# Kernel optimization log

Hardware: AMD Instinct MI355X
Metric: run time of the kernel (lower is better)

Reference implementation:

```python
import jax, jax.numpy as jnp
import numpy as np

B, L, D, H = 8, 1024, 512, 8  # L must equal len_ for the skew trick
DH = D // H


def setup_inputs() -> dict:
    key = jax.random.key(0)
    ks = jax.random.split(key, 6)
    s = 0.02
    return {
        "x": jax.random.normal(ks[0], (B, L, D), dtype=jnp.float32),
        "Wq": jax.random.normal(ks[1], (D, D), dtype=jnp.float32) * s,
        "Wk": jax.random.normal(ks[2], (D, D), dtype=jnp.float32) * s,
        "Wv": jax.random.normal(ks[3], (D, D), dtype=jnp.float32) * s,
        "We": jax.random.normal(ks[4], (L, DH), dtype=jnp.float32) * s,  # e_projection weight: (len_, d_head)
        "Wo": jax.random.normal(ks[5], (D, D), dtype=jnp.float32) * s,
        "bo": jnp.zeros((D,), dtype=jnp.float32),
        "unused": 0,
    }


def reference(x, Wq, Wk, Wv, We, Wo, bo, unused):
    Bx, Lx, Dx = x.shape
    q = (x @ Wq.T).reshape(Bx, Lx, H, DH)  # blhd
    k = (x @ Wk.T).reshape(Bx, Lx, H, DH)
    v = (x @ Wv.T).reshape(Bx, Lx, H, DH)

    # relative-position logits: e_projection(q) then permute -> (B, H, L, len_)
    qe = jnp.einsum('blhd,ed->bhle', q, We)

    # 'skew' trick: reflect-pad right by L-1, zero-pad (right 1, bottom L-1),
    # reshape (B,H,2L-1,2L) -> (B,H,2L,2L-1), slice [:L, L-1:] -> (B,H,L,L)
    qe = jnp.pad(qe, ((0, 0), (0, 0), (0, 0), (0, Lx - 1)), mode='reflect')
    qe = jnp.pad(qe, ((0, 0), (0, 0), (0, Lx - 1), (0, 1)))
    qe = qe.reshape(Bx, H, 2 * Lx, 2 * Lx - 1)
    s_rel = qe[:, :, :Lx, Lx - 1:]

    scale = 1.0 / jnp.sqrt(jnp.asarray(DH, dtype=x.dtype))
    scores = jnp.einsum('blhd,bshd->bhls', q, k)
    A = jax.nn.softmax(scale * (scores + s_rel), axis=-1)
    V = jnp.einsum('bhls,bshd->blhd', A, v).reshape(Bx, Lx, Dx)
    return V @ Wo.T + bo
```

## Files before the change

kernel.cpp:

```cpp
#include <hip/hip_runtime.h>

#define Lc 1024
#define Dc 512
#define Hc 8
#define DHc 64

typedef __attribute__((ext_vector_type(8))) short bf16x8;
typedef __attribute__((ext_vector_type(4))) float f32x4;

typedef __attribute__((address_space(1))) const unsigned int guint;
typedef __attribute__((address_space(3))) unsigned int luint;

__device__ __forceinline__ void gload_lds16(const void* g, void* l) {
    __builtin_amdgcn_global_load_lds((guint*)g, (luint*)l, 16, 0, 0);
}

__device__ __forceinline__ unsigned short f2bf(float f) {
    unsigned u = __float_as_uint(f);
    u += 0x7fffu + ((u >> 16) & 1u);
    return (unsigned short)(u >> 16);
}
__device__ __forceinline__ unsigned short f2bft(float f) {
    return (unsigned short)(__float_as_uint(f) >> 16);
}
__device__ __forceinline__ unsigned pk2(float a, float b) {
    return (unsigned)f2bf(a) | ((unsigned)f2bf(b) << 16);
}
__device__ __forceinline__ float bf2f(unsigned short s) { return __uint_as_float(((unsigned)s) << 16); }

__global__ void cvt_all_kernel(
    const float* __restrict__ x,  const float* __restrict__ Wq,
    const float* __restrict__ Wk, const float* __restrict__ Wv,
    const float* __restrict__ Wo, const float* __restrict__ We,
    unsigned short* __restrict__ xb,  unsigned short* __restrict__ wqb,
    unsigned short* __restrict__ wkb, unsigned short* __restrict__ wvb,
    unsigned short* __restrict__ wob, unsigned short* __restrict__ wet)
{
    int bid = blockIdx.x;
    const float* src; unsigned short* dst; size_t base;
    if      (bid < 4096) { src = x;  dst = xb;  base = (size_t)bid * 1024; }
    else if (bid < 4352) { src = Wq; dst = wqb; base = (size_t)(bid-4096) * 1024; }
    else if (bid < 4608) { src = Wk; dst = wkb; base = (size_t)(bid-4352) * 1024; }
    else if (bid < 4864) { src = Wv; dst = wvb; base = (size_t)(bid-4608) * 1024; }
    else if (bid < 5120) { src = Wo; dst = wob; base = (size_t)(bid-4864) * 1024; }
    else                 { src = We; dst = wet; base = (size_t)(bid-5120) * 1024; }
    size_t i = base + (size_t)threadIdx.x * 4;
    float4 a = *(const float4*)&src[i];
    *(uint2*)&dst[i] = make_uint2(pk2(a.x, a.y), pk2(a.z, a.w));
}

__global__ __launch_bounds__(256, 3) void proj_mfma_kernel(
    const unsigned short* __restrict__ xb,
    const unsigned short* __restrict__ wq, const unsigned short* __restrict__ wk,
    const unsigned short* __restrict__ wv,
    unsigned short* __restrict__ qo, unsigned short* __restrict__ ko,
    unsigned short* __restrict__ vtg, float qscale)
{
    const unsigned short* W;
    if (blockIdx.z == 0)      W = wq;
    else if (blockIdx.z == 1) W = wk;
    else                      W = wv;

    __shared__ unsigned short smem[128 * 136];
    unsigned short* As = smem;
    unsigned short* Bs = smem + 8192;

    const int t = threadIdx.x;
    const int lane = t & 63, w = t >> 6;
    const int lq = lane >> 4, ln = lane & 15;
    const int m0 = blockIdx.y * 128, n0 = blockIdx.x * 128;
    const int wm = (w & 1) * 64, wn = (w >> 1) * 64;
    const int srow = t >> 3;
    const int lsg  = ((t & 7) ^ ((t >> 3) & 7)) * 8;
    const int key  = ln & 7;

    f32x4 acc[4][4];
    #pragma unroll
    for (int i = 0; i < 4; i++)
        #pragma unroll
        for (int j = 0; j < 4; j++) acc[i][j] = (f32x4){0.f,0.f,0.f,0.f};

    for (int c0 = 0; c0 < 512; c0 += 64) {
        __syncthreads();
        #pragma unroll
        for (int g = 0; g < 4; g++) {
            gload_lds16(&xb[(size_t)(m0 + 32*g + srow) * 512 + c0 + lsg], &As[(32*g + srow)*64 + (t&7)*8]);
            gload_lds16(&W [(size_t)(n0 + 32*g + srow) * 512 + c0 + lsg], &Bs[(32*g + srow)*64 + (t&7)*8]);
        }
        __syncthreads();

        #pragma unroll
        for (int kk = 0; kk < 2; kk++) {
            bf16x8 af[4], bf[4];
            #pragma unroll
            for (int i = 0; i < 4; i++)
                af[i] = *(bf16x8*)&As[(wm + 16*i + ln)*64 + ((kk*4 + lq) ^ key)*8];
            #pragma unroll
            for (int j = 0; j < 4; j++)
                bf[j] = *(bf16x8*)&Bs[(wn + 16*j + ln)*64 + ((kk*4 + lq) ^ key)*8];
            #pragma unroll
            for (int i = 0; i < 4; i++)
                #pragma unroll
                for (int j = 0; j < 4; j++)
                    acc[i][j] = __builtin_amdgcn_mfma_f32_16x16x32_bf16(af[i], bf[j], acc[i][j], 0, 0, 0);
        }
    }

    if (blockIdx.z < 2) {
        unsigned short* out = (blockIdx.z == 0) ? qo : ko;
        const float osc = (blockIdx.z == 0) ? qscale : 1.0f;
        #pragma unroll
        for (int i = 0; i < 4; i++) {
            #pragma unroll
            for (int r = 0; r < 4; r++) {
                int m = m0 + wm + 16*i + 4*lq + r;
                int b = m >> 10, l = m & 1023;
                #pragma unroll
                for (int j = 0; j < 4; j++) {
                    int n = n0 + wn + 16*j + ln;
                    int h = n >> 6, dh = n & 63;
                    out[((size_t)((b*Hc + h)*Lc + l))*DHc + dh] = f2bf(acc[i][j][r] * osc);
                }
            }
        }
    } else {
        __syncthreads();
        unsigned short* Ts = smem;
        #pragma unroll
        for (int i = 0; i < 4; i++) {
            int mlb = wm + 16*i + 4*lq;
            #pragma unroll
            for (int j = 0; j < 4; j++) {
                int nl = wn + 16*j + ln;
                *(uint2*)&Ts[nl*136 + mlb] = make_uint2(pk2(acc[i][j][0], acc[i][j][1]),
                                                        pk2(acc[i][j][2], acc[i][j][3]));
            }
        }
        __syncthreads();
        const int b = m0 >> 10, l0m = m0 & 1023;
        const int nl = t >> 1, seg = (t & 1) * 64;
        const int ng = n0 + nl, h = ng >> 6, dh = ng & 63;
        unsigned short* dst = vtg + (((size_t)(b*Hc + h))*DHc + dh)*Lc + l0m + seg;
        #pragma unroll
        for (int u = 0; u < 8; u++)
            *(uint4*)&dst[8*u] = *(uint4*)&Ts[nl*136 + seg + 8*u];
    }
}

__global__ __launch_bounds__(256, 4) void out_mfma_kernel(
    const unsigned short* __restrict__ A, const unsigned short* __restrict__ W,
    const float* __restrict__ bias, float* __restrict__ out)
{
    __shared__ unsigned short As[64 * 64];
    __shared__ unsigned short Bs[64 * 64];

    const int t = threadIdx.x;
    const int lane = t & 63, w = t >> 6;
    const int lq = lane >> 4, ln = lane & 15;
    const int m0 = blockIdx.y * 64, n0 = blockIdx.x * 64;
    const int wm = (w & 1) * 32, wn = (w >> 1) * 32;
    const int srow = t >> 3;
    const int lsg  = ((t & 7) ^ ((t >> 3) & 7)) * 8;
    const int key  = ln & 7;

    f32x4 acc[2][2];
    #pragma unroll
    for (int i = 0; i < 2; i++)
        #pragma unroll
        for (int j = 0; j < 2; j++) acc[i][j] = (f32x4){0.f,0.f,0.f,0.f};

    for (int c0 = 0; c0 < 512; c0 += 64) {
        __syncthreads();
        #pragma unroll
        for (int g = 0; g < 2; g++) {
            gload_lds16(&A[(size_t)(m0 + 32*g + srow) * 512 + c0 + lsg], &As[(32*g + srow)*64 + (t&7)*8]);
            gload_lds16(&W[(size_t)(n0 + 32*g + srow) * 512 + c0 + lsg], &Bs[(32*g + srow)*64 + (t&7)*8]);
        }
        __syncthreads();

        #pragma unroll
        for (int kk = 0; kk < 2; kk++) {
            bf16x8 af[2], bf[2];
            #pragma unroll
            for (int i = 0; i < 2; i++)
                af[i] = *(bf16x8*)&As[(wm + 16*i + ln)*64 + ((kk*4 + lq) ^ key)*8];
            #pragma unroll
            for (int j = 0; j < 2; j++)
                bf[j] = *(bf16x8*)&Bs[(wn + 16*j + ln)*64 + ((kk*4 + lq) ^ key)*8];
            #pragma unroll
            for (int i = 0; i < 2; i++)
                #pragma unroll
                for (int j = 0; j < 2; j++)
                    acc[i][j] = __builtin_amdgcn_mfma_f32_16x16x32_bf16(af[i], bf[j], acc[i][j], 0, 0, 0);
        }
    }

    float bb[2];
    #pragma unroll
    for (int j = 0; j < 2; j++) bb[j] = bias[n0 + wn + 16*j + ln];

    #pragma unroll
    for (int i = 0; i < 2; i++) {
        #pragma unroll
        for (int r = 0; r < 4; r++) {
            int m = m0 + wm + 16*i + 4*lq + r;
            #pragma unroll
            for (int j = 0; j < 2; j++) {
                int n = n0 + wn + 16*j + ln;
                out[(size_t)m * Dc + n] = acc[i][j][r] + bb[j];
            }
        }
    }
}

__global__ __launch_bounds__(256, 4) void attn_v7_kernel(
    const unsigned short* __restrict__ q, const unsigned short* __restrict__ k,
    const unsigned short* __restrict__ vtg, const unsigned short* __restrict__ wet,
    unsigned short* __restrict__ attn)
{
    __shared__ unsigned short ksp [2 * 64 * 32];
    __shared__ unsigned short vtp [2 * 64 * 32];
    __shared__ unsigned short ps  [2 * 64 * 32];
    __shared__ unsigned short qes [128 * 64];

    unsigned short* wesp = ps;

    const int t    = threadIdx.x;
    const int lane = t & 63, w = t >> 6;
    const int lq   = lane >> 4, ln = lane & 15;
    const int wr   = (w >> 1) * 32;
    const int wc   = w & 1;

    const int n   = blockIdx.x;
    const int xcd = n & 7, idx = n >> 3;
    const int bh  = xcd * 8 + (idx >> 4);
    const int l0  = (idx & 15) * 64;

    const unsigned short* qb  = q   + (size_t)bh * (Lc * DHc);
    const unsigned short* kb  = k   + (size_t)bh * (Lc * DHc);
    const unsigned short* vtb = vtg + (size_t)bh * (DHc * Lc);

    const int trow = t >> 2;
    const int sseg = ((t & 3) ^ ((t >> 4) & 3)) * 8;
    const int swz  = (ln >> 2) & 3;

    const bf16x8 onesf = {(short)0x3F80,(short)0x3F80,(short)0x3F80,(short)0x3F80,
                          (short)0x3F80,(short)0x3F80,(short)0x3F80,(short)0x3F80};

    bf16x8 qa[2][2];
    #pragma unroll
    for (int rg = 0; rg < 2; rg++)
        #pragma unroll
        for (int kk = 0; kk < 2; kk++)
            qa[rg][kk] = *(const bf16x8*)&qb[(size_t)(l0 + wr + 16*rg + ln)*64 + kk*32 + lq*8];

    const int pb0 = 15 - (l0 >> 6);
    gload_lds16(&wet[(size_t)(64*pb0 + trow)*64 +      sseg], &wesp[t*8]);
    gload_lds16(&wet[(size_t)(64*pb0 + trow)*64 + 32 + sseg], &wesp[2048 + t*8]);
    __syncthreads();
    {
        f32x4 qec[2][2];
        #pragma unroll
        for (int rg = 0; rg < 2; rg++)
            #pragma unroll
            for (int ct = 0; ct < 2; ct++) qec[rg][ct] = (f32x4){0.f,0.f,0.f,0.f};
        #pragma unroll
        for (int kk = 0; kk < 2; kk++)
            #pragma unroll
            for (int ct = 0; ct < 2; ct++) {
                bf16x8 bf = *(bf16x8*)&wesp[kk*2048 + (16*(2*wc+ct) + ln)*32 + (lq ^ swz)*8];
                #pragma unroll
                for (int rg = 0; rg < 2; rg++)
                    qec[rg][ct] = __builtin_amdgcn_mfma_f32_16x16x32_bf16(qa[rg][kk], bf, qec[rg][ct], 0, 0, 0);
            }
        const int cb = (pb0 & 1) * 64;
        #pragma unroll
        for (int ct = 0; ct < 2; ct++) {
            const int row = cb + 16*(2*wc+ct) + ln;
            #pragma unroll
            for (int rg = 0; rg < 2; rg++)
                *(uint2*)&qes[row*64 + ((wr + 16*rg + 4*lq) ^ (ln << 2))] =
                    make_uint2(pk2(qec[rg][ct][0], qec[rg][ct][1]),
                               pk2(qec[rg][ct][2], qec[rg][ct][3]));
        }
    }

    f32x4 Lacc[2];
    f32x4 Ov[2][2];
    #pragma unroll
    for (int rg = 0; rg < 2; rg++) {
        Lacc[rg] = (f32x4){0.f,0.f,0.f,0.f};
        #pragma unroll
        for (int ct = 0; ct < 2; ct++) Ov[rg][ct] = (f32x4){0.f,0.f,0.f,0.f};
    }

    int pbOld = pb0 - 1;

    for (int s0 = 0; s0 < Lc; s0 += 64) {
        const int c0  = l0 - s0;
        const int ac0 = c0 < 0 ? -c0 : c0;
        const int pb  = (960 - ac0) >> 6;
        const int newp = (pb > pbOld) ? pb + 1 : pb;
        pbOld = pb;
        const int cb = (newp & 1) * 64;

        __syncthreads();
        gload_lds16(&kb [(size_t)(s0 + trow)*64 +      sseg], &ksp [t*8]);
        gload_lds16(&kb [(size_t)(s0 + trow)*64 + 32 + sseg], &ksp [2048 + t*8]);
        gload_lds16(&vtb[(size_t)trow*1024 + s0 +      sseg], &vtp [t*8]);
        gload_lds16(&vtb[(size_t)trow*1024 + s0 + 32 + sseg], &vtp [2048 + t*8]);
        gload_lds16(&wet[(size_t)(64*newp + trow)*64 +      sseg], &wesp[t*8]);
        gload_lds16(&wet[(size_t)(64*newp + trow)*64 + 32 + sseg], &wesp[2048 + t*8]);
        __syncthreads();

        {
            f32x4 qec[2][2];
            #pragma unroll
            for (int rg = 0; rg < 2; rg++)
                #pragma unroll
                for (int ct = 0; ct < 2; ct++) qec[rg][ct] = (f32x4){0.f,0.f,0.f,0.f};
            #pragma unroll
            for (int kk = 0; kk < 2; kk++)
                #pragma unroll
                for (int ct = 0; ct < 2; ct++) {
                    bf16x8 bf = *(bf16x8*)&wesp[kk*2048 + (16*(2*wc+ct) + ln)*32 + (lq ^ swz)*8];
                    #pragma unroll
                    for (int rg = 0; rg < 2; rg++)
                        qec[rg][ct] = __builtin_amdgcn_mfma_f32_16x16x32_bf16(qa[rg][kk], bf, qec[rg][ct], 0, 0, 0);
                }
            #pragma unroll
            for (int ct = 0; ct < 2; ct++) {
                const int row = cb + 16*(2*wc+ct) + ln;
                #pragma unroll
                for (int rg = 0; rg < 2; rg++)
                    *(uint2*)&qes[row*64 + ((wr + 16*rg + 4*lq) ^ (ln << 2))] =
                        make_uint2(pk2(qec[rg][ct][0], qec[rg][ct][1]),
                                   pk2(qec[rg][ct][2], qec[rg][ct][3]));
            }
        }

        __syncthreads();

        f32x4 sc[2][2];
        #pragma unroll
        for (int rg = 0; rg < 2; rg++)
            #pragma unroll
            for (int ct = 0; ct < 2; ct++) sc[rg][ct] = (f32x4){0.f,0.f,0.f,0.f};
        #pragma unroll
        for (int kk = 0; kk < 2; kk++)
            #pragma unroll
            for (int ct = 0; ct < 2; ct++) {
                bf16x8 bfk = *(bf16x8*)&ksp[kk*2048 + (16*(2*wc+ct) + ln)*32 + (lq ^ swz)*8];
                #pragma unroll
                for (int rg = 0; rg < 2; rg++)
                    sc[rg][ct] = __builtin_amdgcn_mfma_f32_16x16x32_bf16(qa[rg][kk], bfk, sc[rg][ct], 0, 0, 0);
            }

        #pragma unroll
        for (int rg = 0; rg < 2; rg++)
            #pragma unroll
            for (int r = 0; r < 4; r++) {
                const int lr = wr + 16*rg + 4*lq + r;
                const int dbase = c0 + lr - ln;
                #pragma unroll
                for (int ct = 0; ct < 2; ct++) {
                    int d  = dbase - 16*(2*wc+ct);
                    int ad = d < 0 ? -d : d;
                    int m  = 1023 - ad;
                    float bias = bf2f(qes[(m & 127)*64 + (lr ^ ((m & 15) << 2))]);
                    float pv = __builtin_amdgcn_exp2f(sc[rg][ct][r] + bias);
                    int seg = ((ct*2 + (ln >> 3)) ^ lq);
                    ps[wc*2048 + lr*32 + seg*8 + (ln & 7)] = f2bft(pv);
                }
            }

        __syncthreads();

        #pragma unroll
        for (int kk = 0; kk < 2; kk++) {
            bf16x8 pa[2];
            #pragma unroll
            for (int rg = 0; rg < 2; rg++)
                pa[rg] = *(bf16x8*)&ps[kk*2048 + (wr + 16*rg + ln)*32 + (lq ^ swz)*8];
            #pragma unroll
            for (int rg = 0; rg < 2; rg++)
                Lacc[rg] = __builtin_amdgcn_mfma_f32_16x16x32_bf16(pa[rg], onesf, Lacc[rg], 0, 0, 0);
            #pragma unroll
            for (int ct = 0; ct < 2; ct++) {
                bf16x8 vf = *(bf16x8*)&vtp[kk*2048 + (16*(2*wc+ct) + ln)*32 + (lq ^ swz)*8];
                #pragma unroll
                for (int rg = 0; rg < 2; rg++)
                    Ov[rg][ct] = __builtin_amdgcn_mfma_f32_16x16x32_bf16(pa[rg], vf, Ov[rg][ct], 0, 0, 0);
            }
        }
    }

    const int b = bh >> 3, h = bh & 7;
    #pragma unroll
    for (int rg = 0; rg < 2; rg++)
        #pragma unroll
        for (int r = 0; r < 4; r++) {
            float inv = 1.f / Lacc[rg][r];
            int l = l0 + wr + 16*rg + 4*lq + r;
            #pragma unroll
            for (int ct = 0; ct < 2; ct++)
                attn[((size_t)(b*Lc + l))*Dc + h*DHc + 16*(2*wc+ct) + ln] = f2bf(Ov[rg][ct][r] * inv);
        }
}

extern "C" void kernel_launch(void* const* d_in, const int* in_sizes, int n_in,
                              void* d_out, int out_size, void* d_ws, size_t ws_size,
                              hipStream_t stream)
{
    (void)in_sizes; (void)n_in; (void)out_size; (void)ws_size;
    const float* x  = (const float*)d_in[0];
    const float* Wq = (const float*)d_in[1];
    const float* Wk = (const float*)d_in[2];
    const float* Wv = (const float*)d_in[3];
    const float* We = (const float*)d_in[4];
    const float* Wo = (const float*)d_in[5];
    const float* bo = (const float*)d_in[6];

    const size_t NT = (size_t)8 * Hc * Lc * DHc;
    unsigned short* qw  = (unsigned short*)d_ws;
    unsigned short* kw  = qw  + NT;
    unsigned short* vtg = kw  + NT;
    unsigned short* xbf = vtg + NT;
    unsigned short* awb = xbf + NT;
    unsigned short* wqb = awb + NT;
    unsigned short* wkb = wqb + 262144;
    unsigned short* wvb = wkb + 262144;
    unsigned short* wob = wvb + 262144;
    unsigned short* wet = wob + 262144;

    cvt_all_kernel<<<5184, 256, 0, stream>>>(x, Wq, Wk, Wv, Wo, We,
                                             xbf, wqb, wkb, wvb, wob, wet);
    proj_mfma_kernel<<<dim3(4, 64, 3), 256, 0, stream>>>(xbf, wqb, wkb, wvb,
                                                         qw, kw, vtg,
                                                         0.125f * 1.44269504089f);
    attn_v7_kernel<<<1024, 256, 0, stream>>>(qw, kw, vtg, wet, awb);
    out_mfma_kernel<<<dim3(8, 128), 256, 0, stream>>>(awb, wob, bo, (float*)d_out);
}
```

Before: 173.8 us.

## Load K, V and We MFMA fragments directly from global instead of LDS staging

```diff
diff --git a/kernel.cpp b/kernel.cpp
--- a/kernel.cpp
+++ b/kernel.cpp
@@ -213,17 +213,13 @@
     }
 }
 
-__global__ __launch_bounds__(256, 4) void attn_v7_kernel(
+__global__ __launch_bounds__(256, 4) void attn_v8_kernel(
     const unsigned short* __restrict__ q, const unsigned short* __restrict__ k,
     const unsigned short* __restrict__ vtg, const unsigned short* __restrict__ wet,
     unsigned short* __restrict__ attn)
 {
-    __shared__ unsigned short ksp [2 * 64 * 32];
-    __shared__ unsigned short vtp [2 * 64 * 32];
     __shared__ unsigned short ps  [2 * 64 * 32];
     __shared__ unsigned short qes [128 * 64];
-
-    unsigned short* wesp = ps;
 
     const int t    = threadIdx.x;
     const int lane = t & 63, w = t >> 6;
@@ -240,8 +236,6 @@
     const unsigned short* kb  = k   + (size_t)bh * (Lc * DHc);
     const unsigned short* vtb = vtg + (size_t)bh * (DHc * Lc);
 
-    const int trow = t >> 2;
-    const int sseg = ((t & 3) ^ ((t >> 4) & 3)) * 8;
     const int swz  = (ln >> 2) & 3;
 
     const bf16x8 onesf = {(short)0x3F80,(short)0x3F80,(short)0x3F80,(short)0x3F80,
@@ -255,9 +249,6 @@
             qa[rg][kk] = *(const bf16x8*)&qb[(size_t)(l0 + wr + 16*rg + ln)*64 + kk*32 + lq*8];
 
     const int pb0 = 15 - (l0 >> 6);
-    gload_lds16(&wet[(size_t)(64*pb0 + trow)*64 +      sseg], &wesp[t*8]);
-    gload_lds16(&wet[(size_t)(64*pb0 + trow)*64 + 32 + sseg], &wesp[2048 + t*8]);
-    __syncthreads();
     {
         f32x4 qec[2][2];
         #pragma unroll
@@ -268,7 +259,7 @@
         for (int kk = 0; kk < 2; kk++)
             #pragma unroll
             for (int ct = 0; ct < 2; ct++) {
-                bf16x8 bf = *(bf16x8*)&wesp[kk*2048 + (16*(2*wc+ct) + ln)*32 + (lq ^ swz)*8];
+                bf16x8 bf = *(const bf16x8*)&wet[(size_t)(64*pb0 + 16*(2*wc+ct) + ln)*64 + kk*32 + lq*8];
                 #pragma unroll
                 for (int rg = 0; rg < 2; rg++)
                     qec[rg][ct] = __builtin_amdgcn_mfma_f32_16x16x32_bf16(qa[rg][kk], bf, qec[rg][ct], 0, 0, 0);
@@ -304,14 +295,15 @@
         pbOld = pb;
         const int cb = (newp & 1) * 64;
 
-        __syncthreads();
-        gload_lds16(&kb [(size_t)(s0 + trow)*64 +      sseg], &ksp [t*8]);
-        gload_lds16(&kb [(size_t)(s0 + trow)*64 + 32 + sseg], &ksp [2048 + t*8]);
-        gload_lds16(&vtb[(size_t)trow*1024 + s0 +      sseg], &vtp [t*8]);
-        gload_lds16(&vtb[(size_t)trow*1024 + s0 + 32 + sseg], &vtp [2048 + t*8]);
-        gload_lds16(&wet[(size_t)(64*newp + trow)*64 +      sseg], &wesp[t*8]);
-        gload_lds16(&wet[(size_t)(64*newp + trow)*64 + 32 + sseg], &wesp[2048 + t*8]);
-        __syncthreads();
+        bf16x8 wfr[2][2], kfr[2][2];
+        #pragma unroll
+        for (int kk = 0; kk < 2; kk++)
+            #pragma unroll
+            for (int ct = 0; ct < 2; ct++) {
+                const int row = 16*(2*wc+ct) + ln;
+                wfr[kk][ct] = *(const bf16x8*)&wet[(size_t)(64*newp + row)*64 + kk*32 + lq*8];
+                kfr[kk][ct] = *(const bf16x8*)&kb [(size_t)(s0 + row)*64 + kk*32 + lq*8];
+            }
 
         {
             f32x4 qec[2][2];
@@ -322,12 +314,10 @@
             #pragma unroll
             for (int kk = 0; kk < 2; kk++)
                 #pragma unroll
-                for (int ct = 0; ct < 2; ct++) {
-                    bf16x8 bf = *(bf16x8*)&wesp[kk*2048 + (16*(2*wc+ct) + ln)*32 + (lq ^ swz)*8];
+                for (int ct = 0; ct < 2; ct++)
                     #pragma unroll
                     for (int rg = 0; rg < 2; rg++)
-                        qec[rg][ct] = __builtin_amdgcn_mfma_f32_16x16x32_bf16(qa[rg][kk], bf, qec[rg][ct], 0, 0, 0);
-                }
+                        qec[rg][ct] = __builtin_amdgcn_mfma_f32_16x16x32_bf16(qa[rg][kk], wfr[kk][ct], qec[rg][ct], 0, 0, 0);
             #pragma unroll
             for (int ct = 0; ct < 2; ct++) {
                 const int row = cb + 16*(2*wc+ct) + ln;
@@ -341,6 +331,13 @@
 
         __syncthreads();
 
+        bf16x8 vfr[2][2];
+        #pragma unroll
+        for (int kk = 0; kk < 2; kk++)
+            #pragma unroll
+            for (int ct = 0; ct < 2; ct++)
+                vfr[kk][ct] = *(const bf16x8*)&vtb[(size_t)(16*(2*wc+ct) + ln)*1024 + s0 + kk*32 + lq*8];
+
         f32x4 sc[2][2];
         #pragma unroll
         for (int rg = 0; rg < 2; rg++)
@@ -349,12 +346,10 @@
         #pragma unroll
         for (int kk = 0; kk < 2; kk++)
             #pragma unroll
-            for (int ct = 0; ct < 2; ct++) {
-                bf16x8 bfk = *(bf16x8*)&ksp[kk*2048 + (16*(2*wc+ct) + ln)*32 + (lq ^ swz)*8];
+            for (int ct = 0; ct < 2; ct++)
                 #pragma unroll
                 for (int rg = 0; rg < 2; rg++)
-                    sc[rg][ct] = __builtin_amdgcn_mfma_f32_16x16x32_bf16(qa[rg][kk], bfk, sc[rg][ct], 0, 0, 0);
-            }
+                    sc[rg][ct] = __builtin_amdgcn_mfma_f32_16x16x32_bf16(qa[rg][kk], kfr[kk][ct], sc[rg][ct], 0, 0, 0);
 
         #pragma unroll
         for (int rg = 0; rg < 2; rg++)
@@ -386,12 +381,10 @@
             for (int rg = 0; rg < 2; rg++)
                 Lacc[rg] = __builtin_amdgcn_mfma_f32_16x16x32_bf16(pa[rg], onesf, Lacc[rg], 0, 0, 0);
             #pragma unroll
-            for (int ct = 0; ct < 2; ct++) {
-                bf16x8 vf = *(bf16x8*)&vtp[kk*2048 + (16*(2*wc+ct) + ln)*32 + (lq ^ swz)*8];
+            for (int ct = 0; ct < 2; ct++)
                 #pragma unroll
                 for (int rg = 0; rg < 2; rg++)
-                    Ov[rg][ct] = __builtin_amdgcn_mfma_f32_16x16x32_bf16(pa[rg], vf, Ov[rg][ct], 0, 0, 0);
-            }
+                    Ov[rg][ct] = __builtin_amdgcn_mfma_f32_16x16x32_bf16(pa[rg], vfr[kk][ct], Ov[rg][ct], 0, 0, 0);
         }
     }
 
@@ -438,6 +431,6 @@
     proj_mfma_kernel<<<dim3(4, 64, 3), 256, 0, stream>>>(xbf, wqb, wkb, wvb,
                                                          qw, kw, vtg,
                                                          0.125f * 1.44269504089f);
-    attn_v7_kernel<<<1024, 256, 0, stream>>>(qw, kw, vtg, wet, awb);
+    attn_v8_kernel<<<1024, 256, 0, stream>>>(qw, kw, vtg, wet, awb);
     out_mfma_kernel<<<dim3(8, 128), 256, 0, stream>>>(awb, wob, bo, (float*)d_out);
 }
```

Result: slower. 203.3 us (+17.0%).

## Compute transposed score tiles so P is packed and stored as vectors

Applied to the files above, without the earlier changes.

```diff
diff --git a/kernel.cpp b/kernel.cpp
--- a/kernel.cpp
+++ b/kernel.cpp
@@ -20,11 +20,11 @@
     u += 0x7fffu + ((u >> 16) & 1u);
     return (unsigned short)(u >> 16);
 }
-__device__ __forceinline__ unsigned short f2bft(float f) {
-    return (unsigned short)(__float_as_uint(f) >> 16);
-}
 __device__ __forceinline__ unsigned pk2(float a, float b) {
     return (unsigned)f2bf(a) | ((unsigned)f2bf(b) << 16);
+}
+__device__ __forceinline__ unsigned pk2t(float a, float b) {
+    return __builtin_amdgcn_perm(__float_as_uint(b), __float_as_uint(a), 0x07060302u);
 }
 __device__ __forceinline__ float bf2f(unsigned short s) { return __uint_as_float(((unsigned)s) << 16); }
 
@@ -213,23 +213,23 @@
     }
 }
 
-__global__ __launch_bounds__(256, 4) void attn_v7_kernel(
+__global__ __launch_bounds__(256, 4) void attn_v9_kernel(
     const unsigned short* __restrict__ q, const unsigned short* __restrict__ k,
     const unsigned short* __restrict__ vtg, const unsigned short* __restrict__ wet,
     unsigned short* __restrict__ attn)
 {
     __shared__ unsigned short ksp [2 * 64 * 32];
     __shared__ unsigned short vtp [2 * 64 * 32];
-    __shared__ unsigned short ps  [2 * 64 * 32];
+    __shared__ unsigned short ps2 [64 * 64];
     __shared__ unsigned short qes [128 * 64];
 
-    unsigned short* wesp = ps;
+    unsigned short* wesp = ps2;
 
     const int t    = threadIdx.x;
     const int lane = t & 63, w = t >> 6;
     const int lq   = lane >> 4, ln = lane & 15;
-    const int wr   = (w >> 1) * 32;
-    const int wc   = w & 1;
+    const int si   = w >> 1;
+    const int li   = w & 1;
 
     const int n   = blockIdx.x;
     const int xcd = n & 7, idx = n >> 3;
@@ -247,12 +247,12 @@
     const bf16x8 onesf = {(short)0x3F80,(short)0x3F80,(short)0x3F80,(short)0x3F80,
                           (short)0x3F80,(short)0x3F80,(short)0x3F80,(short)0x3F80};
 
-    bf16x8 qa[2][2];
-    #pragma unroll
-    for (int rg = 0; rg < 2; rg++)
+    bf16x8 qf[2][2];
+    #pragma unroll
+    for (int lt = 0; lt < 2; lt++)
         #pragma unroll
         for (int kk = 0; kk < 2; kk++)
-            qa[rg][kk] = *(const bf16x8*)&qb[(size_t)(l0 + wr + 16*rg + ln)*64 + kk*32 + lq*8];
+            qf[lt][kk] = *(const bf16x8*)&qb[(size_t)(l0 + 32*li + 16*lt + ln)*64 + kk*32 + lq*8];
 
     const int pb0 = 15 - (l0 >> 6);
     gload_lds16(&wet[(size_t)(64*pb0 + trow)*64 +      sseg], &wesp[t*8]);
@@ -261,37 +261,37 @@
     {
         f32x4 qec[2][2];
         #pragma unroll
-        for (int rg = 0; rg < 2; rg++)
-            #pragma unroll
-            for (int ct = 0; ct < 2; ct++) qec[rg][ct] = (f32x4){0.f,0.f,0.f,0.f};
+        for (int lt = 0; lt < 2; lt++)
+            #pragma unroll
+            for (int et = 0; et < 2; et++) qec[lt][et] = (f32x4){0.f,0.f,0.f,0.f};
         #pragma unroll
         for (int kk = 0; kk < 2; kk++)
             #pragma unroll
-            for (int ct = 0; ct < 2; ct++) {
-                bf16x8 bf = *(bf16x8*)&wesp[kk*2048 + (16*(2*wc+ct) + ln)*32 + (lq ^ swz)*8];
-                #pragma unroll
-                for (int rg = 0; rg < 2; rg++)
-                    qec[rg][ct] = __builtin_amdgcn_mfma_f32_16x16x32_bf16(qa[rg][kk], bf, qec[rg][ct], 0, 0, 0);
+            for (int et = 0; et < 2; et++) {
+                bf16x8 wf = *(bf16x8*)&wesp[kk*2048 + (16*(2*si+et) + ln)*32 + (lq ^ swz)*8];
+                #pragma unroll
+                for (int lt = 0; lt < 2; lt++)
+                    qec[lt][et] = __builtin_amdgcn_mfma_f32_16x16x32_bf16(qf[lt][kk], wf, qec[lt][et], 0, 0, 0);
             }
         const int cb = (pb0 & 1) * 64;
         #pragma unroll
-        for (int ct = 0; ct < 2; ct++) {
-            const int row = cb + 16*(2*wc+ct) + ln;
-            #pragma unroll
-            for (int rg = 0; rg < 2; rg++)
-                *(uint2*)&qes[row*64 + ((wr + 16*rg + 4*lq) ^ (ln << 2))] =
-                    make_uint2(pk2(qec[rg][ct][0], qec[rg][ct][1]),
-                               pk2(qec[rg][ct][2], qec[rg][ct][3]));
+        for (int et = 0; et < 2; et++) {
+            const int row = cb + 16*(2*si+et) + ln;
+            #pragma unroll
+            for (int lt = 0; lt < 2; lt++)
+                *(uint2*)&qes[row*64 + ((32*li + 16*lt + 4*lq) ^ (ln << 2))] =
+                    make_uint2(pk2(qec[lt][et][0], qec[lt][et][1]),
+                               pk2(qec[lt][et][2], qec[lt][et][3]));
         }
     }
 
     f32x4 Lacc[2];
     f32x4 Ov[2][2];
     #pragma unroll
-    for (int rg = 0; rg < 2; rg++) {
-        Lacc[rg] = (f32x4){0.f,0.f,0.f,0.f};
-        #pragma unroll
-        for (int ct = 0; ct < 2; ct++) Ov[rg][ct] = (f32x4){0.f,0.f,0.f,0.f};
+    for (int lt = 0; lt < 2; lt++) {
+        Lacc[lt] = (f32x4){0.f,0.f,0.f,0.f};
+        #pragma unroll
+        for (int dt = 0; dt < 2; dt++) Ov[dt][lt] = (f32x4){0.f,0.f,0.f,0.f};
     }
 
     int pbOld = pb0 - 1;
@@ -316,26 +316,26 @@
         {
             f32x4 qec[2][2];
             #pragma unroll
-            for (int rg = 0; rg < 2; rg++)
-                #pragma unroll
-                for (int ct = 0; ct < 2; ct++) qec[rg][ct] = (f32x4){0.f,0.f,0.f,0.f};
+            for (int lt = 0; lt < 2; lt++)
+                #pragma unroll
+                for (int et = 0; et < 2; et++) qec[lt][et] = (f32x4){0.f,0.f,0.f,0.f};
             #pragma unroll
             for (int kk = 0; kk < 2; kk++)
                 #pragma unroll
-                for (int ct = 0; ct < 2; ct++) {
-                    bf16x8 bf = *(bf16x8*)&wesp[kk*2048 + (16*(2*wc+ct) + ln)*32 + (lq ^ swz)*8];
+                for (int et = 0; et < 2; et++) {
+                    bf16x8 wf = *(bf16x8*)&wesp[kk*2048 + (16*(2*si+et) + ln)*32 + (lq ^ swz)*8];
                     #pragma unroll
-                    for (int rg = 0; rg < 2; rg++)
-                        qec[rg][ct] = __builtin_amdgcn_mfma_f32_16x16x32_bf16(qa[rg][kk], bf, qec[rg][ct], 0, 0, 0);
+                    for (int lt = 0; lt < 2; lt++)
+                        qec[lt][et] = __builtin_amdgcn_mfma_f32_16x16x32_bf16(qf[lt][kk], wf, qec[lt][et], 0, 0, 0);
                 }
             #pragma unroll
-            for (int ct = 0; ct < 2; ct++) {
-                const int row = cb + 16*(2*wc+ct) + ln;
-                #pragma unroll
-                for (int rg = 0; rg < 2; rg++)
-                    *(uint2*)&qes[row*64 + ((wr + 16*rg + 4*lq) ^ (ln << 2))] =
-                        make_uint2(pk2(qec[rg][ct][0], qec[rg][ct][1]),
-                                   pk2(qec[rg][ct][2], qec[rg][ct][3]));
+            for (int et = 0; et < 2; et++) {
+                const int row = cb + 16*(2*si+et) + ln;
+                #pragma unroll
+                for (int lt = 0; lt < 2; lt++)
+                    *(uint2*)&qes[row*64 + ((32*li + 16*lt + 4*lq) ^ (ln << 2))] =
+                        make_uint2(pk2(qec[lt][et][0], qec[lt][et][1]),
+                                   pk2(qec[lt][et][2], qec[lt][et][3]));
             }
         }
 
@@ -343,69 +343,75 @@
 
         f32x4 sc[2][2];
         #pragma unroll
-        for (int rg = 0; rg < 2; rg++)
-            #pragma unroll
-            for (int ct = 0; ct < 2; ct++) sc[rg][ct] = (f32x4){0.f,0.f,0.f,0.f};
+        for (int st = 0; st < 2; st++)
+            #pragma unroll
+            for (int lt = 0; lt < 2; lt++) sc[st][lt] = (f32x4){0.f,0.f,0.f,0.f};
         #pragma unroll
         for (int kk = 0; kk < 2; kk++)
             #pragma unroll
-            for (int ct = 0; ct < 2; ct++) {
-                bf16x8 bfk = *(bf16x8*)&ksp[kk*2048 + (16*(2*wc+ct) + ln)*32 + (lq ^ swz)*8];
-                #pragma unroll
-                for (int rg = 0; rg < 2; rg++)
-                    sc[rg][ct] = __builtin_amdgcn_mfma_f32_16x16x32_bf16(qa[rg][kk], bfk, sc[rg][ct], 0, 0, 0);
-            }
-
-        #pragma unroll
-        for (int rg = 0; rg < 2; rg++)
-            #pragma unroll
-            for (int r = 0; r < 4; r++) {
-                const int lr = wr + 16*rg + 4*lq + r;
-                const int dbase = c0 + lr - ln;
-                #pragma unroll
-                for (int ct = 0; ct < 2; ct++) {
-                    int d  = dbase - 16*(2*wc+ct);
+            for (int st = 0; st < 2; st++) {
+                bf16x8 kf = *(bf16x8*)&ksp[kk*2048 + (32*si + 16*st + ln)*32 + (lq ^ swz)*8];
+                #pragma unroll
+                for (int lt = 0; lt < 2; lt++)
+                    sc[st][lt] = __builtin_amdgcn_mfma_f32_16x16x32_bf16(kf, qf[lt][kk], sc[st][lt], 0, 0, 0);
+            }
+
+        #pragma unroll
+        for (int st = 0; st < 2; st++)
+            #pragma unroll
+            for (int lt = 0; lt < 2; lt++) {
+                const int lloc = 32*li + 16*lt + ln;
+                const int sb   = 32*si + 16*st + 4*lq;
+                float p[4];
+                #pragma unroll
+                for (int r = 0; r < 4; r++) {
+                    int d  = c0 + lloc - (sb + r);
                     int ad = d < 0 ? -d : d;
                     int m  = 1023 - ad;
-                    float bias = bf2f(qes[(m & 127)*64 + (lr ^ ((m & 15) << 2))]);
-                    float pv = __builtin_amdgcn_exp2f(sc[rg][ct][r] + bias);
-                    int seg = ((ct*2 + (ln >> 3)) ^ lq);
-                    ps[wc*2048 + lr*32 + seg*8 + (ln & 7)] = f2bft(pv);
+                    float bias = bf2f(qes[(m & 127)*64 + (lloc ^ ((m & 15) << 2))]);
+                    p[r] = __builtin_amdgcn_exp2f(sc[st][lt][r] + bias);
                 }
+                const int blk = (4*si + 2*st + (lq >> 1)) ^ (ln & 7);
+                *(uint2*)&ps2[lloc*64 + blk*8 + (lq & 1)*4] =
+                    make_uint2(pk2t(p[0], p[1]), pk2t(p[2], p[3]));
             }
 
         __syncthreads();
 
         #pragma unroll
         for (int kk = 0; kk < 2; kk++) {
-            bf16x8 pa[2];
-            #pragma unroll
-            for (int rg = 0; rg < 2; rg++)
-                pa[rg] = *(bf16x8*)&ps[kk*2048 + (wr + 16*rg + ln)*32 + (lq ^ swz)*8];
-            #pragma unroll
-            for (int rg = 0; rg < 2; rg++)
-                Lacc[rg] = __builtin_amdgcn_mfma_f32_16x16x32_bf16(pa[rg], onesf, Lacc[rg], 0, 0, 0);
-            #pragma unroll
-            for (int ct = 0; ct < 2; ct++) {
-                bf16x8 vf = *(bf16x8*)&vtp[kk*2048 + (16*(2*wc+ct) + ln)*32 + (lq ^ swz)*8];
-                #pragma unroll
-                for (int rg = 0; rg < 2; rg++)
-                    Ov[rg][ct] = __builtin_amdgcn_mfma_f32_16x16x32_bf16(pa[rg], vf, Ov[rg][ct], 0, 0, 0);
+            bf16x8 pf[2];
+            #pragma unroll
+            for (int lt = 0; lt < 2; lt++) {
+                const int row = 32*li + 16*lt + ln;
+                pf[lt] = *(bf16x8*)&ps2[row*64 + ((4*kk + lq) ^ (ln & 7))*8];
+            }
+            #pragma unroll
+            for (int lt = 0; lt < 2; lt++)
+                Lacc[lt] = __builtin_amdgcn_mfma_f32_16x16x32_bf16(onesf, pf[lt], Lacc[lt], 0, 0, 0);
+            #pragma unroll
+            for (int dt = 0; dt < 2; dt++) {
+                bf16x8 vf = *(bf16x8*)&vtp[kk*2048 + (32*si + 16*dt + ln)*32 + (lq ^ swz)*8];
+                #pragma unroll
+                for (int lt = 0; lt < 2; lt++)
+                    Ov[dt][lt] = __builtin_amdgcn_mfma_f32_16x16x32_bf16(vf, pf[lt], Ov[dt][lt], 0, 0, 0);
             }
         }
     }
 
     const int b = bh >> 3, h = bh & 7;
     #pragma unroll
-    for (int rg = 0; rg < 2; rg++)
-        #pragma unroll
-        for (int r = 0; r < 4; r++) {
-            float inv = 1.f / Lacc[rg][r];
-            int l = l0 + wr + 16*rg + 4*lq + r;
-            #pragma unroll
-            for (int ct = 0; ct < 2; ct++)
-                attn[((size_t)(b*Lc + l))*Dc + h*DHc + 16*(2*wc+ct) + ln] = f2bf(Ov[rg][ct][r] * inv);
-        }
+    for (int lt = 0; lt < 2; lt++) {
+        const float inv = 1.f / Lacc[lt][0];
+        const int l = l0 + 32*li + 16*lt + ln;
+        unsigned short* dst = &attn[((size_t)(b*Lc + l))*Dc + h*DHc];
+        #pragma unroll
+        for (int dt = 0; dt < 2; dt++) {
+            const int dh = 32*si + 16*dt + 4*lq;
+            *(uint2*)&dst[dh] = make_uint2(pk2(Ov[dt][lt][0]*inv, Ov[dt][lt][1]*inv),
+                                           pk2(Ov[dt][lt][2]*inv, Ov[dt][lt][3]*inv));
+        }
+    }
 }
 
 extern "C" void kernel_launch(void* const* d_in, const int* in_sizes, int n_in,
@@ -438,6 +444,6 @@
     proj_mfma_kernel<<<dim3(4, 64, 3), 256, 0, stream>>>(xbf, wqb, wkb, wvb,
                                                          qw, kw, vtg,
                                                          0.125f * 1.44269504089f);
-    attn_v7_kernel<<<1024, 256, 0, stream>>>(qw, kw, vtg, wet, awb);
+    attn_v9_kernel<<<1024, 256, 0, stream>>>(qw, kw, vtg, wet, awb);
     out_mfma_kernel<<<dim3(8, 128), 256, 0, stream>>>(awb, wob, bo, (float*)d_out);
 }
```

New measurement: 170.6 us. No clear change (-1.8%).
